# Kernel tuning notes

Hardware: AMD Instinct MI355X
Metric: run time of the kernel (lower is better)

Reference implementation:

```python
import jax, jax.numpy as jnp
import numpy as np

NORM_EPS = 1e-6

B, C, H, W = 4, 256, 48, 48
CE = 512           # C * expansion_ratio
N_STATE = 16       # Mamba d_state
DT_RANK = 32       # Ce // 16


def setup_inputs() -> dict:
    key = jax.random.key(0)
    ks = jax.random.split(key, 12)
    s = 0.02
    inp = {
        "x": jax.random.normal(ks[0], (B, C, H, W), jnp.float32),
        "norm_w": jnp.ones((C,), jnp.float32),
        "norm_b": jnp.zeros((C,), jnp.float32),
        "w_ex": jax.random.normal(ks[1], (2 * CE, C), jnp.float32) * s,
        "b_ex": jnp.zeros((2 * CE,), jnp.float32),
        "w_proj": jax.random.normal(ks[2], (C, CE), jnp.float32) * s,
        "b_proj": jnp.zeros((C,), jnp.float32),
        "dw_kernel": jax.random.normal(ks[3], (3, 3, 1, CE), jnp.float32) * 0.1,  # HWIO depthwise
        "A_log": jnp.log(jnp.broadcast_to(jnp.arange(1, N_STATE + 1, dtype=jnp.float32), (CE, N_STATE))),
        "D": jnp.ones((CE,), jnp.float32),
        "W_xproj": jax.random.normal(ks[4], (DT_RANK + 2 * N_STATE, CE), jnp.float32) * s,
        "b_xproj": jnp.zeros((DT_RANK + 2 * N_STATE,), jnp.float32),
        "W_dt": jax.random.normal(ks[5], (CE, DT_RANK), jnp.float32) * s,
        "b_dt": jnp.full((CE,), -3.0, jnp.float32),  # softplus -> small positive dt
    }
    return inp


def _forward(x, norm_w, norm_b, w_ex, b_ex, w_proj, b_proj,
             dw_kernel, A_log, D, W_xproj, b_xproj, W_dt, b_dt):
    Bt, Cc, Hh, Ww = x.shape
    Ce = dw_kernel.shape[-1]
    Ns = A_log.shape[1]
    dt_rank = W_dt.shape[1]

    # NCHW -> NHWC, LayerNorm over C
    xp = jnp.transpose(x, (0, 2, 3, 1))
    mu = xp.mean(-1, keepdims=True)
    var = xp.var(-1, keepdims=True)
    xn = (xp - mu) * jax.lax.rsqrt(var + NORM_EPS) * norm_w + norm_b

    # expansion + split
    uv = xn @ w_ex.T + b_ex                       # [B,H,W,2Ce]
    u, v = jnp.split(uv, 2, axis=-1)
    gate = u * jax.nn.sigmoid(-u)                 # r_silu(u)
    g = u * jax.nn.sigmoid(u)                     # SiLU(u)

    # depthwise 3x3 conv (NHWC) + SiLU
    v = jax.lax.conv_general_dilated(
        v, dw_kernel, window_strides=(1, 1), padding='SAME',
        dimension_numbers=('NHWC', 'HWIO', 'NHWC'), feature_group_count=Ce)
    v = v * jax.nn.sigmoid(v)

    gate = v * gate                               # fuse gate before SSM

    # ---- Mamba selective scan over raster-flattened HW sequence ----
    L = Hh * Ww
    vs = v.reshape(Bt, L, Ce)                     # [B,L,Ce]
    dbc = vs @ W_xproj.T + b_xproj                # [B,L,dt_rank+2N]
    dt = dbc[..., :dt_rank]
    Bm = dbc[..., dt_rank:dt_rank + Ns]           # [B,L,N]
    Cm = dbc[..., dt_rank + Ns:]                  # [B,L,N]
    delta = jax.nn.softplus(dt @ W_dt.T + b_dt)   # [B,L,Ce]
    A = -jnp.exp(A_log)                           # [Ce,N], negative -> stable

    def step(h, inp):
        d_t, b_t, c_t, v_t = inp                  # [B,Ce],[B,N],[B,N],[B,Ce]
        dA = jnp.exp(d_t[..., None] * A)          # [B,Ce,N]
        h = h * dA + d_t[..., None] * b_t[:, None, :] * v_t[..., None]
        y = jnp.einsum('bcn,bn->bc', h, c_t) + D * v_t
        return h, y

    h0 = jnp.zeros((Bt, Ce, Ns), x.dtype)
    seq = (jnp.swapaxes(delta, 0, 1), jnp.swapaxes(Bm, 0, 1),
           jnp.swapaxes(Cm, 0, 1), jnp.swapaxes(vs, 0, 1))
    _, ys = jax.lax.scan(step, h0, seq)           # ys: [L,B,Ce]
    y = jnp.swapaxes(ys, 0, 1).reshape(Bt, Hh, Ww, Ce)

    out = (y * g + gate) @ w_proj.T + b_proj      # [B,H,W,C]
    return jnp.transpose(out, (0, 3, 1, 2))       # NCHW


def reference(x, norm_w, norm_b, w_ex, b_ex, w_proj, b_proj,
              dw_kernel, A_log, D, W_xproj, b_xproj, W_dt, b_dt):
    return _forward(x, norm_w, norm_b, w_ex, b_ex, w_proj, b_proj,
                    dw_kernel, A_log, D, W_xproj, b_xproj, W_dt, b_dt)
```

## Files before the change

kernel.cpp:

```cpp
#include <hip/hip_runtime.h>
#include <hip/hip_bf16.h>

#define B_   4
#define C_   256
#define HH   48
#define WW   48
#define L_   2304
#define BL   9216
#define CE_  512
#define NS   16
#define DTR  32
#define NCH  72
#define CHL  32

typedef __attribute__((ext_vector_type(8))) short s16x8;
typedef __attribute__((ext_vector_type(4))) float f32x4;

__device__ __forceinline__ ushort f2bf(float f) {
  union { float f; unsigned u; } v; v.f = f;
  unsigned r = v.u + 0x7fffu + ((v.u >> 16) & 1u);
  return (ushort)(r >> 16);
}
__device__ __forceinline__ float bf2f(ushort h) {
  union { unsigned u; float f; } v; v.u = ((unsigned)h) << 16;
  return v.f;
}
__device__ __forceinline__ float lo_f(unsigned u) {
  union { unsigned u; float f; } v; v.u = u << 16; return v.f;
}
__device__ __forceinline__ float hi_f(unsigned u) {
  union { unsigned u; float f; } v; v.u = u & 0xffff0000u; return v.f;
}

__global__ __launch_bounds__(256) void prep_k(const float* __restrict__ w_ex,
                                              const float* __restrict__ w_proj,
                                              const float* __restrict__ W_xp,
                                              const float* __restrict__ b_xp,
                                              const float* __restrict__ W_dt,
                                              const float* __restrict__ b_dt,
                                              ushort* __restrict__ w_ex_bf,
                                              ushort* __restrict__ w_proj_bf,
                                              ushort* __restrict__ wcat_bf,
                                              float* __restrict__ bcat) {
  int idx = blockIdx.x * 256 + threadIdx.x;
  if (idx < 262144) {
    w_ex_bf[idx] = f2bf(w_ex[idx]);
  } else if (idx < 393216) {
    int i = idx - 262144; w_proj_bf[i] = f2bf(w_proj[i]);
  } else if (idx < 688128) {
    int i2 = idx - 393216;
    int i = i2 >> 9, j = i2 & 511;
    float s = 0.f;
    if (i < 512) {
      #pragma unroll
      for (int r = 0; r < 32; r++) s = fmaf(W_dt[i * 32 + r], W_xp[r * 512 + j], s);
    } else if (i < 544) {
      s = W_xp[(i - 480) * 512 + j];
    }
    wcat_bf[i2] = f2bf(s);
  } else if (idx < 688704) {
    int n = idx - 688128;
    float s;
    if (n < 512) {
      s = b_dt[n];
      #pragma unroll
      for (int r = 0; r < 32; r++) s = fmaf(W_dt[n * 32 + r], b_xp[r], s);
    } else if (n < 544) {
      s = b_xp[32 + (n - 512)];
    } else s = 0.f;
    bcat[n] = s;
  }
}

__global__ __launch_bounds__(256) void ln_k(const float* __restrict__ x,
                                            const float* __restrict__ w,
                                            const float* __restrict__ bia,
                                            ushort* __restrict__ xn_bf) {
  __shared__ float xt[C_][17];
  __shared__ float ps[16][17], ps2[16][17];
  __shared__ float mu_s[16], r_s[16];
  __shared__ float w_s[C_], b_s[C_];
  int blk = blockIdx.x;
  int b = blk / 144, p0 = (blk - b * 144) * 16;
  int t = threadIdx.x;
  w_s[t] = w[t]; b_s[t] = bia[t];
  #pragma unroll
  for (int it = 0; it < 16; it++) {
    int i = it * 256 + t;
    int c = i >> 4, pj = i & 15;
    xt[c][pj] = x[((size_t)(b * C_ + c)) * L_ + p0 + pj];
  }
  __syncthreads();
  {
    int ci = t >> 4, pj = t & 15;
    float s = 0.f, s2 = 0.f;
    #pragma unroll
    for (int k = 0; k < 16; k++) {
      float v = xt[ci * 16 + k][pj];
      s += v; s2 += v * v;
    }
    ps[ci][pj] = s; ps2[ci][pj] = s2;
  }
  __syncthreads();
  if (t < 16) {
    float s = 0.f, s2 = 0.f;
    #pragma unroll
    for (int ci = 0; ci < 16; ci++) { s += ps[ci][t]; s2 += ps2[ci][t]; }
    float mu = s * (1.f / C_);
    float var = s2 * (1.f / C_) - mu * mu;
    mu_s[t] = mu; r_s[t] = rsqrtf(var + 1e-6f);
  }
  __syncthreads();
  int pj = t & 15, c0 = (t >> 4) * 16;
  float mu = mu_s[pj], r = r_s[pj];
  s16x8 v0, v1;
  #pragma unroll
  for (int k = 0; k < 8; k++) {
    int c = c0 + k;
    v0[k] = (short)f2bf((xt[c][pj] - mu) * r * w_s[c] + b_s[c]);
  }
  #pragma unroll
  for (int k = 0; k < 8; k++) {
    int c = c0 + 8 + k;
    v1[k] = (short)f2bf((xt[c][pj] - mu) * r * w_s[c] + b_s[c]);
  }
  ushort* dst = xn_bf + ((size_t)(b * L_ + p0 + pj)) * C_ + c0;
  *(s16x8*)dst = v0;
  *(s16x8*)(dst + 8) = v1;
}

template<int TM, int TN, int WN, int FM, int FN, int K>
__device__ __forceinline__ void mfma_gemm(const ushort* __restrict__ A,
                                          const ushort* __restrict__ Bm,
                                          int m0, int n0, ushort* sh,
                                          f32x4 acc[FM][FN]) {
  const int t = threadIdx.x;
  const int lane = t & 63;
  const int wid = t >> 6;
  const int wm = wid / WN, wn = wid % WN;
  constexpr int ASZ = TM * 32, BSZ = TN * 32;
  #pragma unroll
  for (int i = 0; i < FM; i++)
    #pragma unroll
    for (int j = 0; j < FN; j++) acc[i][j] = (f32x4){0.f, 0.f, 0.f, 0.f};

  auto stage = [&](int kt, int buf) {
    ushort* Ad = sh + buf * (ASZ + BSZ);
    ushort* Bd = Ad + ASZ;
    #pragma unroll
    for (int ch = t; ch < TM * 4; ch += 256) {
      int k8 = ch / TM, row = ch % TM;
      const ushort* g = A + (size_t)(m0 + row) * K + kt + k8 * 8;
      __builtin_amdgcn_global_load_lds(
          (const __attribute__((address_space(1))) void*)g,
          (__attribute__((address_space(3))) void*)(Ad + (k8 * TM + row) * 8), 16, 0, 0);
    }
    #pragma unroll
    for (int ch = t; ch < TN * 4; ch += 256) {
      int k8 = ch / TN, row = ch % TN;
      const ushort* g = Bm + (size_t)(n0 + row) * K + kt + k8 * 8;
      __builtin_amdgcn_global_load_lds(
          (const __attribute__((address_space(1))) void*)g,
          (__attribute__((address_space(3))) void*)(Bd + (k8 * TN + row) * 8), 16, 0, 0);
    }
  };

  stage(0, 0);
  __syncthreads();
  constexpr int NK = K / 32;
  const int k8 = lane >> 4, r = lane & 15;
  #pragma unroll
  for (int kt = 0; kt < NK; kt++) {
    const int cur = kt & 1;
    if (kt + 1 < NK) stage((kt + 1) * 32, cur ^ 1);
    const ushort* Ab = sh + cur * (ASZ + BSZ);
    const ushort* Bb = Ab + ASZ;
    s16x8 a[FM], b[FN];
    #pragma unroll
    for (int i = 0; i < FM; i++)
      a[i] = *(const s16x8*)(Ab + (k8 * TM + wm * FM * 16 + i * 16 + r) * 8);
    #pragma unroll
    for (int j = 0; j < FN; j++)
      b[j] = *(const s16x8*)(Bb + (k8 * TN + wn * FN * 16 + j * 16 + r) * 8);
    #pragma unroll
    for (int i = 0; i < FM; i++)
      #pragma unroll
      for (int j = 0; j < FN; j++)
        acc[i][j] = __builtin_amdgcn_mfma_f32_16x16x32_bf16(a[i], b[j], acc[i][j], 0, 0, 0);
    __syncthreads();
  }
}

__global__ __launch_bounds__(256) void gemm_expand_k(const ushort* __restrict__ xn,
                                                     const ushort* __restrict__ wex,
                                                     const float* __restrict__ b_ex,
                                                     ushort* __restrict__ u_bf,
                                                     ushort* __restrict__ v_bf) {
  __shared__ __align__(16) ushort sh[128 * 136];
  f32x4 acc[4][4];
  int m0 = blockIdx.y * 128, n0 = blockIdx.x * 128;
  mfma_gemm<128, 128, 2, 4, 4, 256>(xn, wex, m0, n0, sh, acc);
  int lane = threadIdx.x & 63, wid = threadIdx.x >> 6;
  int wm = wid >> 1, wn = wid & 1;
  int q4 = (lane >> 4) * 4, cix = lane & 15;
  const int ST = 136;
  #pragma unroll
  for (int j = 0; j < 4; j++) {
    int ncl = wn * 64 + j * 16 + cix;
    float bias = b_ex[n0 + ncl];
    #pragma unroll
    for (int i = 0; i < 4; i++) {
      int ml = wm * 64 + i * 16 + q4;
      #pragma unroll
      for (int q = 0; q < 4; q++)
        sh[(ml + q) * ST + ncl] = f2bf(acc[i][j][q] + bias);
    }
  }
  __syncthreads();
  ushort* base = (n0 < 512) ? u_bf : v_bf;
  int nb = (n0 < 512) ? n0 : n0 - 512;
  int ml = threadIdx.x >> 1, nc0 = (threadIdx.x & 1) * 64;
  ushort* dst = base + (size_t)(m0 + ml) * CE_ + nb + nc0;
  const ushort* srcp = sh + ml * ST + nc0;
  #pragma unroll
  for (int k = 0; k < 8; k++)
    *(s16x8*)(dst + k * 8) = *(const s16x8*)(srcp + k * 8);
}

__global__ __launch_bounds__(256) void gemm_dbc_k(const ushort* __restrict__ vs,
                                                  const ushort* __restrict__ wcat,
                                                  const float* __restrict__ bcat,
                                                  float* __restrict__ delta,
                                                  float* __restrict__ bc) {
  __shared__ __align__(16) ushort sh[2 * (128 * 32 + 64 * 32)];
  f32x4 acc[4][2];
  int m0 = blockIdx.y * 128, n0 = blockIdx.x * 64;
  mfma_gemm<128, 64, 2, 4, 2, 512>(vs, wcat, m0, n0, sh, acc);
  int lane = threadIdx.x & 63, wid = threadIdx.x >> 6;
  int wm = wid >> 1, wn = wid & 1;
  int q4 = (lane >> 4) * 4, cix = lane & 15;
  #pragma unroll
  for (int j = 0; j < 2; j++) {
    int nc = n0 + wn * 32 + j * 16 + cix;
    if (nc >= 544) continue;
    float bias = bcat[nc];
    #pragma unroll
    for (int i = 0; i < 4; i++) {
      int mr = m0 + wm * 64 + i * 16 + q4;
      #pragma unroll
      for (int q = 0; q < 4; q++) {
        float xv = acc[i][j][q] + bias;
        if (nc < 512)
          delta[(size_t)(mr + q) * CE_ + nc] =
              fmaxf(xv, 0.f) + __logf(1.f + __expf(-fabsf(xv)));
        else
          bc[(size_t)(mr + q) * 32 + (nc - 512)] = xv;
      }
    }
  }
}

__global__ __launch_bounds__(256) void gemm_proj_k(const ushort* __restrict__ z,
                                                   const ushort* __restrict__ wpr,
                                                   const float* __restrict__ b_proj,
                                                   float* __restrict__ out) {
  __shared__ __align__(16) ushort sh[2 * (64 * 32 + 64 * 32)];
  __shared__ float Cs[64][65];
  f32x4 acc[2][2];
  int m0 = blockIdx.y * 64, n0 = blockIdx.x * 64;
  mfma_gemm<64, 64, 2, 2, 2, 512>(z, wpr, m0, n0, sh, acc);
  int t = threadIdx.x;
  int lane = t & 63, wid = t >> 6;
  int wm = wid >> 1, wn = wid & 1;
  int q4 = (lane >> 4) * 4, cix = lane & 15;
  #pragma unroll
  for (int j = 0; j < 2; j++)
    #pragma unroll
    for (int i = 0; i < 2; i++)
      #pragma unroll
      for (int q = 0; q < 4; q++)
        Cs[wm * 32 + i * 16 + q4 + q][wn * 32 + j * 16 + cix] = acc[i][j][q];
  __syncthreads();
  int nc_l = t >> 2, p4 = (t & 3) * 16;
  float bias = b_proj[n0 + nc_l];
  int pix0 = m0 + p4;
  int bb = pix0 / L_, p = pix0 - bb * L_;
  float* dst = out + ((size_t)(bb * C_ + n0 + nc_l)) * L_ + p;
  #pragma unroll
  for (int k = 0; k < 4; k++) {
    float4 vv = make_float4(Cs[p4 + k * 4 + 0][nc_l] + bias,
                            Cs[p4 + k * 4 + 1][nc_l] + bias,
                            Cs[p4 + k * 4 + 2][nc_l] + bias,
                            Cs[p4 + k * 4 + 3][nc_l] + bias);
    *(float4*)(dst + k * 4) = vv;
  }
}

__global__ __launch_bounds__(256) void dwconv_k(const ushort* __restrict__ vraw,
                                                const float* __restrict__ kw,
                                                ushort* __restrict__ vs) {
  int p = blockIdx.x * 2 + (threadIdx.x >> 7);
  int b = p / L_, q = p - b * L_;
  int y = q / WW, x = q - y * WW;
  int c4 = (threadIdx.x & 127) * 4;
  float a0 = 0.f, a1 = 0.f, a2 = 0.f, a3 = 0.f;
  #pragma unroll
  for (int ky = 0; ky < 3; ky++) {
    int yy = y + ky - 1;
    if (yy < 0 || yy >= HH) continue;
    #pragma unroll
    for (int kx = 0; kx < 3; kx++) {
      int xx = x + kx - 1;
      if (xx < 0 || xx >= WW) continue;
      uint2 pv = *(const uint2*)(vraw + ((size_t)(b * L_ + yy * WW + xx)) * CE_ + c4);
      float4 kk = *(const float4*)(kw + (ky * 3 + kx) * CE_ + c4);
      a0 = fmaf(lo_f(pv.x), kk.x, a0);
      a1 = fmaf(hi_f(pv.x), kk.y, a1);
      a2 = fmaf(lo_f(pv.y), kk.z, a2);
      a3 = fmaf(hi_f(pv.y), kk.w, a3);
    }
  }
  float s0 = a0 / (1.f + __expf(-a0));
  float s1 = a1 / (1.f + __expf(-a1));
  float s2 = a2 / (1.f + __expf(-a2));
  float s3 = a3 / (1.f + __expf(-a3));
  uint2 outp;
  outp.x = (unsigned)f2bf(s0) | ((unsigned)f2bf(s1) << 16);
  outp.y = (unsigned)f2bf(s2) | ((unsigned)f2bf(s3) << 16);
  *(uint2*)(vs + (size_t)p * CE_ + c4) = outp;
}

__global__ __launch_bounds__(256) void scan1_k(const float* __restrict__ delta,
                                               const float* __restrict__ bc,
                                               const ushort* __restrict__ vs,
                                               const float* __restrict__ A_log,
                                               float* __restrict__ S,
                                               float* __restrict__ Dsum) {
  __shared__ float bt_s[CHL * NS];
  int b = blockIdx.z, ch = blockIdx.y;
  int c = blockIdx.x * 256 + threadIdx.x;
  int mbase = b * L_ + ch * CHL;
  for (int i = threadIdx.x; i < CHL * NS; i += 256)
    bt_s[i] = bc[(size_t)(mbase + (i >> 4)) * 32 + (i & 15)];
  __syncthreads();
  float Ac[NS], h[NS];
  #pragma unroll
  for (int n = 0; n < NS; n++) {
    Ac[n] = -__expf(A_log[c * NS + n]);
    h[n] = 0.f;
  }
  float dsum = 0.f;
  for (int t = 0; t < CHL; t++) {
    int m = mbase + t;
    float d  = delta[(size_t)m * CE_ + c];
    float vv = bf2f(vs[(size_t)m * CE_ + c]);
    float dv = d * vv;
    dsum += d;
    #pragma unroll
    for (int n = 0; n < NS; n++)
      h[n] = fmaf(h[n], __expf(d * Ac[n]), dv * bt_s[t * NS + n]);
  }
  size_t sidx = (size_t)(b * NCH + ch) * CE_ + c;
  #pragma unroll
  for (int n = 0; n < NS; n++) S[sidx * NS + n] = h[n];
  Dsum[sidx] = dsum;
}

__global__ __launch_bounds__(256) void scan2_k(const float* __restrict__ A_log,
                                               float* __restrict__ S,
                                               const float* __restrict__ Dsum) {
  int idx = blockIdx.x * 256 + threadIdx.x;
  int n = idx & 15, c = (idx >> 4) & (CE_ - 1), b = idx >> 13;
  float Ac = -__expf(A_log[c * NS + n]);
  float h = 0.f;
  for (int ch = 0; ch < NCH; ch++) {
    size_t sidx = (size_t)(b * NCH + ch) * CE_ + c;
    float sv = S[sidx * NS + n];
    float ds = Dsum[sidx];
    S[sidx * NS + n] = h;
    h = fmaf(h, __expf(Ac * ds), sv);
  }
}

__global__ __launch_bounds__(256) void scan3_k(const float* __restrict__ delta,
                                               const float* __restrict__ bc,
                                               const ushort* __restrict__ vs,
                                               const float* __restrict__ A_log,
                                               const float* __restrict__ Dv,
                                               const float* __restrict__ hstart,
                                               const ushort* __restrict__ u,
                                               ushort* __restrict__ z) {
  __shared__ float bc_s[CHL * 32];
  int b = blockIdx.z, ch = blockIdx.y;
  int c = blockIdx.x * 256 + threadIdx.x;
  int mbase = b * L_ + ch * CHL;
  for (int i = threadIdx.x; i < CHL * 32; i += 256)
    bc_s[i] = bc[(size_t)(mbase + (i >> 5)) * 32 + (i & 31)];
  __syncthreads();
  size_t sidx = (size_t)(b * NCH + ch) * CE_ + c;
  float Ac[NS], h[NS];
  #pragma unroll
  for (int n = 0; n < NS; n++) {
    Ac[n] = -__expf(A_log[c * NS + n]);
    h[n] = hstart[sidx * NS + n];
  }
  float Dc = Dv[c];
  for (int t = 0; t < CHL; t++) {
    int m = mbase + t;
    float d  = delta[(size_t)m * CE_ + c];
    float vv = bf2f(vs[(size_t)m * CE_ + c]);
    float dv = d * vv;
    float y = 0.f;
    #pragma unroll
    for (int n = 0; n < NS; n++) {
      h[n] = fmaf(h[n], __expf(d * Ac[n]), dv * bc_s[t * 32 + n]);
      y = fmaf(h[n], bc_s[t * 32 + 16 + n], y);
    }
    y = fmaf(Dc, vv, y);
    float uu = bf2f(u[(size_t)m * CE_ + c]);
    float s  = 1.f / (1.f + __expf(-uu));
    z[(size_t)m * CE_ + c] = f2bf(uu * (y * s + vv * (1.f - s)));
  }
}

extern "C" void kernel_launch(void* const* d_in, const int* in_sizes, int n_in,
                              void* d_out, int out_size, void* d_ws, size_t ws_size,
                              hipStream_t stream) {
  const float* x      = (const float*)d_in[0];
  const float* norm_w = (const float*)d_in[1];
  const float* norm_b = (const float*)d_in[2];
  const float* w_ex   = (const float*)d_in[3];
  const float* b_ex   = (const float*)d_in[4];
  const float* w_proj = (const float*)d_in[5];
  const float* b_proj = (const float*)d_in[6];
  const float* dw_k   = (const float*)d_in[7];
  const float* A_log  = (const float*)d_in[8];
  const float* Dv     = (const float*)d_in[9];
  const float* W_xp   = (const float*)d_in[10];
  const float* b_xp   = (const float*)d_in[11];
  const float* W_dt   = (const float*)d_in[12];
  const float* b_dt   = (const float*)d_in[13];
  float* out = (float*)d_out;

  char* wsb = (char*)d_ws;
  size_t off = 0;
  auto alloc = [&](size_t bytes) { void* p = wsb + off; off += (bytes + 255) & ~(size_t)255; return p; };
  ushort* u_bf    = (ushort*)alloc((size_t)BL * CE_ * 2);
  ushort* vraw_bf = (ushort*)alloc((size_t)BL * CE_ * 2);
  ushort* vs_bf   = (ushort*)alloc((size_t)BL * CE_ * 2);
  ushort* xn_bf   = (ushort*)alloc((size_t)BL * C_ * 2);
  float*  delta   = (float*)alloc((size_t)BL * CE_ * 4);
  float*  bc      = (float*)alloc((size_t)BL * 32 * 4);
  float*  S       = (float*)alloc((size_t)B_ * NCH * CE_ * NS * 4);
  float*  Dsum    = (float*)alloc((size_t)B_ * NCH * CE_ * 4);
  ushort* w_ex_bf = (ushort*)alloc((size_t)2 * CE_ * C_ * 2);
  ushort* w_pr_bf = (ushort*)alloc((size_t)C_ * CE_ * 2);
  ushort* wcat_bf = (ushort*)alloc((size_t)576 * CE_ * 2);
  float*  bcat    = (float*)alloc((size_t)576 * 4);
  ushort* z_bf = vraw_bf;

  prep_k<<<2691, 256, 0, stream>>>(w_ex, w_proj, W_xp, b_xp, W_dt, b_dt,
                                   w_ex_bf, w_pr_bf, wcat_bf, bcat);
  ln_k<<<576, 256, 0, stream>>>(x, norm_w, norm_b, xn_bf);
  gemm_expand_k<<<dim3(8, 72), 256, 0, stream>>>(xn_bf, w_ex_bf, b_ex, u_bf, vraw_bf);
  dwconv_k<<<BL / 2, 256, 0, stream>>>(vraw_bf, dw_k, vs_bf);
  gemm_dbc_k<<<dim3(9, 72), 256, 0, stream>>>(vs_bf, wcat_bf, bcat, delta, bc);
  scan1_k<<<dim3(2, NCH, B_), 256, 0, stream>>>(delta, bc, vs_bf, A_log, S, Dsum);
  scan2_k<<<128, 256, 0, stream>>>(A_log, S, Dsum);
  scan3_k<<<dim3(2, NCH, B_), 256, 0, stream>>>(delta, bc, vs_bf, A_log, Dv, S, u_bf, z_bf);
  gemm_proj_k<<<dim3(4, 144), 256, 0, stream>>>(z_bf, w_pr_bf, b_proj, out);
}
```

Measured before the change: 245.6 us.

## Fuse LN with weight prep, bf16 delta, smem-tiled dwconv, swap GEMM grid order

Merges the weight-conversion kernel and the LayerNorm kernel into one launch, and vectorises the LayerNorm loads with float4. Stores delta as bf16, staged through shared memory for coalesced writes, which halves delta traffic in both scan passes; the scan loops are partially unrolled. Rewrites the depthwise conv to stage three input rows and the kernel taps in shared memory per output row. Also swaps the GEMM grid dimensions so M tiles vary fastest. Storing delta in bf16 costs precision in the SSM recurrence.

```diff
diff --git a/kernel.cpp b/kernel.cpp
--- a/kernel.cpp
+++ b/kernel.cpp
@@ -32,101 +32,103 @@
   union { unsigned u; float f; } v; v.u = u & 0xffff0000u; return v.f;
 }
 
-__global__ __launch_bounds__(256) void prep_k(const float* __restrict__ w_ex,
-                                              const float* __restrict__ w_proj,
-                                              const float* __restrict__ W_xp,
-                                              const float* __restrict__ b_xp,
-                                              const float* __restrict__ W_dt,
-                                              const float* __restrict__ b_dt,
-                                              ushort* __restrict__ w_ex_bf,
-                                              ushort* __restrict__ w_proj_bf,
-                                              ushort* __restrict__ wcat_bf,
-                                              float* __restrict__ bcat) {
-  int idx = blockIdx.x * 256 + threadIdx.x;
-  if (idx < 262144) {
-    w_ex_bf[idx] = f2bf(w_ex[idx]);
-  } else if (idx < 393216) {
-    int i = idx - 262144; w_proj_bf[i] = f2bf(w_proj[i]);
-  } else if (idx < 688128) {
-    int i2 = idx - 393216;
-    int i = i2 >> 9, j = i2 & 511;
-    float s = 0.f;
-    if (i < 512) {
-      #pragma unroll
-      for (int r = 0; r < 32; r++) s = fmaf(W_dt[i * 32 + r], W_xp[r * 512 + j], s);
-    } else if (i < 544) {
-      s = W_xp[(i - 480) * 512 + j];
-    }
-    wcat_bf[i2] = f2bf(s);
-  } else if (idx < 688704) {
-    int n = idx - 688128;
-    float s;
-    if (n < 512) {
-      s = b_dt[n];
-      #pragma unroll
-      for (int r = 0; r < 32; r++) s = fmaf(W_dt[n * 32 + r], b_xp[r], s);
-    } else if (n < 544) {
-      s = b_xp[32 + (n - 512)];
-    } else s = 0.f;
-    bcat[n] = s;
-  }
-}
-
-__global__ __launch_bounds__(256) void ln_k(const float* __restrict__ x,
-                                            const float* __restrict__ w,
-                                            const float* __restrict__ bia,
-                                            ushort* __restrict__ xn_bf) {
-  __shared__ float xt[C_][17];
-  __shared__ float ps[16][17], ps2[16][17];
-  __shared__ float mu_s[16], r_s[16];
-  __shared__ float w_s[C_], b_s[C_];
-  int blk = blockIdx.x;
-  int b = blk / 144, p0 = (blk - b * 144) * 16;
+__global__ __launch_bounds__(256) void lnprep_k(const float* __restrict__ x,
+                                                const float* __restrict__ w,
+                                                const float* __restrict__ bia,
+                                                ushort* __restrict__ xn_bf,
+                                                const float* __restrict__ w_ex,
+                                                const float* __restrict__ w_proj,
+                                                const float* __restrict__ W_xp,
+                                                const float* __restrict__ b_xp,
+                                                const float* __restrict__ W_dt,
+                                                const float* __restrict__ b_dt,
+                                                ushort* __restrict__ w_ex_bf,
+                                                ushort* __restrict__ w_proj_bf,
+                                                ushort* __restrict__ wcat_bf,
+                                                float* __restrict__ bcat) {
   int t = threadIdx.x;
-  w_s[t] = w[t]; b_s[t] = bia[t];
-  #pragma unroll
-  for (int it = 0; it < 16; it++) {
-    int i = it * 256 + t;
-    int c = i >> 4, pj = i & 15;
-    xt[c][pj] = x[((size_t)(b * C_ + c)) * L_ + p0 + pj];
-  }
-  __syncthreads();
-  {
-    int ci = t >> 4, pj = t & 15;
-    float s = 0.f, s2 = 0.f;
-    #pragma unroll
-    for (int k = 0; k < 16; k++) {
-      float v = xt[ci * 16 + k][pj];
-      s += v; s2 += v * v;
-    }
-    ps[ci][pj] = s; ps2[ci][pj] = s2;
-  }
-  __syncthreads();
-  if (t < 16) {
-    float s = 0.f, s2 = 0.f;
-    #pragma unroll
-    for (int ci = 0; ci < 16; ci++) { s += ps[ci][t]; s2 += ps2[ci][t]; }
-    float mu = s * (1.f / C_);
-    float var = s2 * (1.f / C_) - mu * mu;
-    mu_s[t] = mu; r_s[t] = rsqrtf(var + 1e-6f);
-  }
-  __syncthreads();
-  int pj = t & 15, c0 = (t >> 4) * 16;
-  float mu = mu_s[pj], r = r_s[pj];
-  s16x8 v0, v1;
-  #pragma unroll
-  for (int k = 0; k < 8; k++) {
-    int c = c0 + k;
-    v0[k] = (short)f2bf((xt[c][pj] - mu) * r * w_s[c] + b_s[c]);
-  }
-  #pragma unroll
-  for (int k = 0; k < 8; k++) {
-    int c = c0 + 8 + k;
-    v1[k] = (short)f2bf((xt[c][pj] - mu) * r * w_s[c] + b_s[c]);
-  }
-  ushort* dst = xn_bf + ((size_t)(b * L_ + p0 + pj)) * C_ + c0;
-  *(s16x8*)dst = v0;
-  *(s16x8*)(dst + 8) = v1;
+  if (blockIdx.x < 576) {
+    __shared__ float xt[C_][17];
+    __shared__ float ps[16][17], ps2[16][17];
+    __shared__ float mu_s[16], r_s[16];
+    __shared__ float w_s[C_], b_s[C_];
+    int blk = blockIdx.x;
+    int b = blk / 144, p0 = (blk - b * 144) * 16;
+    w_s[t] = w[t]; b_s[t] = bia[t];
+    #pragma unroll
+    for (int it = 0; it < 4; it++) {
+      int i = it * 1024 + t * 4;
+      int c = i >> 4, pj = i & 15;
+      float4 v = *(const float4*)&x[((size_t)(b * C_ + c)) * L_ + p0 + pj];
+      xt[c][pj] = v.x; xt[c][pj + 1] = v.y; xt[c][pj + 2] = v.z; xt[c][pj + 3] = v.w;
+    }
+    __syncthreads();
+    {
+      int ci = t >> 4, pj = t & 15;
+      float s = 0.f, s2 = 0.f;
+      #pragma unroll
+      for (int k = 0; k < 16; k++) {
+        float v = xt[ci * 16 + k][pj];
+        s += v; s2 += v * v;
+      }
+      ps[ci][pj] = s; ps2[ci][pj] = s2;
+    }
+    __syncthreads();
+    if (t < 16) {
+      float s = 0.f, s2 = 0.f;
+      #pragma unroll
+      for (int ci = 0; ci < 16; ci++) { s += ps[ci][t]; s2 += ps2[ci][t]; }
+      float mu = s * (1.f / C_);
+      float var = s2 * (1.f / C_) - mu * mu;
+      mu_s[t] = mu; r_s[t] = rsqrtf(var + 1e-6f);
+    }
+    __syncthreads();
+    int pj = t & 15, c0 = (t >> 4) * 16;
+    float mu = mu_s[pj], r = r_s[pj];
+    s16x8 v0, v1;
+    #pragma unroll
+    for (int k = 0; k < 8; k++) {
+      int c = c0 + k;
+      v0[k] = (short)f2bf((xt[c][pj] - mu) * r * w_s[c] + b_s[c]);
+    }
+    #pragma unroll
+    for (int k = 0; k < 8; k++) {
+      int c = c0 + 8 + k;
+      v1[k] = (short)f2bf((xt[c][pj] - mu) * r * w_s[c] + b_s[c]);
+    }
+    ushort* dst = xn_bf + ((size_t)(b * L_ + p0 + pj)) * C_ + c0;
+    *(s16x8*)dst = v0;
+    *(s16x8*)(dst + 8) = v1;
+  } else {
+    int idx = (blockIdx.x - 576) * 256 + t;
+    if (idx < 262144) {
+      w_ex_bf[idx] = f2bf(w_ex[idx]);
+    } else if (idx < 393216) {
+      int i = idx - 262144; w_proj_bf[i] = f2bf(w_proj[i]);
+    } else if (idx < 688128) {
+      int i2 = idx - 393216;
+      int i = i2 >> 9, j = i2 & 511;
+      float s = 0.f;
+      if (i < 512) {
+        #pragma unroll
+        for (int r = 0; r < 32; r++) s = fmaf(W_dt[i * 32 + r], W_xp[r * 512 + j], s);
+      } else if (i < 544) {
+        s = W_xp[(i - 480) * 512 + j];
+      }
+      wcat_bf[i2] = f2bf(s);
+    } else if (idx < 688704) {
+      int n = idx - 688128;
+      float s;
+      if (n < 512) {
+        s = b_dt[n];
+        #pragma unroll
+        for (int r = 0; r < 32; r++) s = fmaf(W_dt[n * 32 + r], b_xp[r], s);
+      } else if (n < 544) {
+        s = b_xp[32 + (n - 512)];
+      } else s = 0.f;
+      bcat[n] = s;
+    }
+  }
 }
 
 template<int TM, int TN, int WN, int FM, int FN, int K>
@@ -198,7 +200,7 @@
                                                      ushort* __restrict__ v_bf) {
   __shared__ __align__(16) ushort sh[128 * 136];
   f32x4 acc[4][4];
-  int m0 = blockIdx.y * 128, n0 = blockIdx.x * 128;
+  int m0 = blockIdx.x * 128, n0 = blockIdx.y * 128;
   mfma_gemm<128, 128, 2, 4, 4, 256>(xn, wex, m0, n0, sh, acc);
   int lane = threadIdx.x & 63, wid = threadIdx.x >> 6;
   int wm = wid >> 1, wn = wid & 1;
@@ -230,31 +232,51 @@
 __global__ __launch_bounds__(256) void gemm_dbc_k(const ushort* __restrict__ vs,
                                                   const ushort* __restrict__ wcat,
                                                   const float* __restrict__ bcat,
-                                                  float* __restrict__ delta,
+                                                  ushort* __restrict__ delta,
                                                   float* __restrict__ bc) {
   __shared__ __align__(16) ushort sh[2 * (128 * 32 + 64 * 32)];
   f32x4 acc[4][2];
-  int m0 = blockIdx.y * 128, n0 = blockIdx.x * 64;
+  int m0 = blockIdx.x * 128, n0 = blockIdx.y * 64;
   mfma_gemm<128, 64, 2, 4, 2, 512>(vs, wcat, m0, n0, sh, acc);
   int lane = threadIdx.x & 63, wid = threadIdx.x >> 6;
   int wm = wid >> 1, wn = wid & 1;
   int q4 = (lane >> 4) * 4, cix = lane & 15;
-  #pragma unroll
-  for (int j = 0; j < 2; j++) {
-    int nc = n0 + wn * 32 + j * 16 + cix;
-    if (nc >= 544) continue;
-    float bias = bcat[nc];
-    #pragma unroll
-    for (int i = 0; i < 4; i++) {
-      int mr = m0 + wm * 64 + i * 16 + q4;
-      #pragma unroll
-      for (int q = 0; q < 4; q++) {
-        float xv = acc[i][j][q] + bias;
-        if (nc < 512)
-          delta[(size_t)(mr + q) * CE_ + nc] =
-              fmaxf(xv, 0.f) + __logf(1.f + __expf(-fabsf(xv)));
-        else
-          bc[(size_t)(mr + q) * 32 + (nc - 512)] = xv;
+  if (n0 < 512) {
+    const int ST = 72;
+    #pragma unroll
+    for (int j = 0; j < 2; j++) {
+      int ncl = wn * 32 + j * 16 + cix;
+      float bias = bcat[n0 + ncl];
+      #pragma unroll
+      for (int i = 0; i < 4; i++) {
+        int ml = wm * 64 + i * 16 + q4;
+        #pragma unroll
+        for (int q = 0; q < 4; q++) {
+          float xv = acc[i][j][q] + bias;
+          float sp = fmaxf(xv, 0.f) + __logf(1.f + __expf(-fabsf(xv)));
+          sh[(ml + q) * ST + ncl] = f2bf(sp);
+        }
+      }
+    }
+    __syncthreads();
+    int ml = threadIdx.x >> 1, h32 = (threadIdx.x & 1) * 32;
+    ushort* dst = delta + (size_t)(m0 + ml) * CE_ + n0 + h32;
+    const ushort* srcp = sh + ml * ST + h32;
+    #pragma unroll
+    for (int k = 0; k < 4; k++)
+      *(s16x8*)(dst + k * 8) = *(const s16x8*)(srcp + k * 8);
+  } else {
+    #pragma unroll
+    for (int j = 0; j < 2; j++) {
+      int nc = n0 + wn * 32 + j * 16 + cix;
+      if (nc >= 544) continue;
+      float bias = bcat[nc];
+      #pragma unroll
+      for (int i = 0; i < 4; i++) {
+        int mr = m0 + wm * 64 + i * 16 + q4;
+        #pragma unroll
+        for (int q = 0; q < 4; q++)
+          bc[(size_t)(mr + q) * 32 + (nc - 512)] = acc[i][j][q] + bias;
       }
     }
   }
@@ -267,7 +289,7 @@
   __shared__ __align__(16) ushort sh[2 * (64 * 32 + 64 * 32)];
   __shared__ float Cs[64][65];
   f32x4 acc[2][2];
-  int m0 = blockIdx.y * 64, n0 = blockIdx.x * 64;
+  int m0 = blockIdx.x * 64, n0 = blockIdx.y * 64;
   mfma_gemm<64, 64, 2, 2, 2, 512>(z, wpr, m0, n0, sh, acc);
   int t = threadIdx.x;
   int lane = t & 63, wid = t >> 6;
@@ -299,38 +321,57 @@
 __global__ __launch_bounds__(256) void dwconv_k(const ushort* __restrict__ vraw,
                                                 const float* __restrict__ kw,
                                                 ushort* __restrict__ vs) {
-  int p = blockIdx.x * 2 + (threadIdx.x >> 7);
-  int b = p / L_, q = p - b * L_;
-  int y = q / WW, x = q - y * WW;
-  int c4 = (threadIdx.x & 127) * 4;
-  float a0 = 0.f, a1 = 0.f, a2 = 0.f, a3 = 0.f;
-  #pragma unroll
-  for (int ky = 0; ky < 3; ky++) {
-    int yy = y + ky - 1;
-    if (yy < 0 || yy >= HH) continue;
-    #pragma unroll
-    for (int kx = 0; kx < 3; kx++) {
-      int xx = x + kx - 1;
-      if (xx < 0 || xx >= WW) continue;
-      uint2 pv = *(const uint2*)(vraw + ((size_t)(b * L_ + yy * WW + xx)) * CE_ + c4);
-      float4 kk = *(const float4*)(kw + (ky * 3 + kx) * CE_ + c4);
-      a0 = fmaf(lo_f(pv.x), kk.x, a0);
-      a1 = fmaf(hi_f(pv.x), kk.y, a1);
-      a2 = fmaf(lo_f(pv.y), kk.z, a2);
-      a3 = fmaf(hi_f(pv.y), kk.w, a3);
-    }
-  }
-  float s0 = a0 / (1.f + __expf(-a0));
-  float s1 = a1 / (1.f + __expf(-a1));
-  float s2 = a2 / (1.f + __expf(-a2));
-  float s3 = a3 / (1.f + __expf(-a3));
-  uint2 outp;
-  outp.x = (unsigned)f2bf(s0) | ((unsigned)f2bf(s1) << 16);
-  outp.y = (unsigned)f2bf(s2) | ((unsigned)f2bf(s3) << 16);
-  *(uint2*)(vs + (size_t)p * CE_ + c4) = outp;
-}
-
-__global__ __launch_bounds__(256) void scan1_k(const float* __restrict__ delta,
+  __shared__ ushort rows[3][WW][128];
+  __shared__ float kws[9][128];
+  int y = blockIdx.x, cg = blockIdx.y, b = blockIdx.z;
+  int t = threadIdx.x;
+  int cbase = cg * 128;
+  for (int i = t; i < 3 * WW * 32; i += 256) {
+    int ry = i / (WW * 32);
+    int rem = i - ry * WW * 32;
+    int xx = rem >> 5, c8 = rem & 31;
+    int yy = y + ry - 1;
+    uint2 val = make_uint2(0u, 0u);
+    if (yy >= 0 && yy < HH)
+      val = *(const uint2*)(vraw + ((size_t)(b * L_ + yy * WW + xx)) * CE_ + cbase + c8 * 4);
+    *(uint2*)&rows[ry][xx][c8 * 4] = val;
+  }
+  for (int i = t; i < 9 * 32; i += 256) {
+    int tap = i >> 5, c8 = i & 31;
+    *(float4*)&kws[tap][c8 * 4] = *(const float4*)(kw + tap * CE_ + cbase + c8 * 4);
+  }
+  __syncthreads();
+  int xg = t >> 5, c8 = t & 31;
+  #pragma unroll
+  for (int xi = 0; xi < 6; xi++) {
+    int x = xg * 6 + xi;
+    float a0 = 0.f, a1 = 0.f, a2 = 0.f, a3 = 0.f;
+    #pragma unroll
+    for (int ky = 0; ky < 3; ky++) {
+      #pragma unroll
+      for (int kx = 0; kx < 3; kx++) {
+        int xx = x + kx - 1;
+        if (xx < 0 || xx >= WW) continue;
+        uint2 pv = *(const uint2*)&rows[ky][xx][c8 * 4];
+        float4 kk = *(const float4*)&kws[ky * 3 + kx][c8 * 4];
+        a0 = fmaf(lo_f(pv.x), kk.x, a0);
+        a1 = fmaf(hi_f(pv.x), kk.y, a1);
+        a2 = fmaf(lo_f(pv.y), kk.z, a2);
+        a3 = fmaf(hi_f(pv.y), kk.w, a3);
+      }
+    }
+    float s0 = a0 / (1.f + __expf(-a0));
+    float s1 = a1 / (1.f + __expf(-a1));
+    float s2 = a2 / (1.f + __expf(-a2));
+    float s3 = a3 / (1.f + __expf(-a3));
+    uint2 outp;
+    outp.x = (unsigned)f2bf(s0) | ((unsigned)f2bf(s1) << 16);
+    outp.y = (unsigned)f2bf(s2) | ((unsigned)f2bf(s3) << 16);
+    *(uint2*)(vs + ((size_t)(b * L_ + y * WW + x)) * CE_ + cbase + c8 * 4) = outp;
+  }
+}
+
+__global__ __launch_bounds__(256) void scan1_k(const ushort* __restrict__ delta,
                                                const float* __restrict__ bc,
                                                const ushort* __restrict__ vs,
                                                const float* __restrict__ A_log,
@@ -350,9 +391,10 @@
     h[n] = 0.f;
   }
   float dsum = 0.f;
+  #pragma unroll 4
   for (int t = 0; t < CHL; t++) {
     int m = mbase + t;
-    float d  = delta[(size_t)m * CE_ + c];
+    float d  = bf2f(delta[(size_t)m * CE_ + c]);
     float vv = bf2f(vs[(size_t)m * CE_ + c]);
     float dv = d * vv;
     dsum += d;
@@ -382,7 +424,7 @@
   }
 }
 
-__global__ __launch_bounds__(256) void scan3_k(const float* __restrict__ delta,
+__global__ __launch_bounds__(256) void scan3_k(const ushort* __restrict__ delta,
                                                const float* __restrict__ bc,
                                                const ushort* __restrict__ vs,
                                                const float* __restrict__ A_log,
@@ -405,9 +447,10 @@
     h[n] = hstart[sidx * NS + n];
   }
   float Dc = Dv[c];
+  #pragma unroll 4
   for (int t = 0; t < CHL; t++) {
     int m = mbase + t;
-    float d  = delta[(size_t)m * CE_ + c];
+    float d  = bf2f(delta[(size_t)m * CE_ + c]);
     float vv = bf2f(vs[(size_t)m * CE_ + c]);
     float dv = d * vv;
     float y = 0.f;
@@ -449,7 +492,7 @@
   ushort* vraw_bf = (ushort*)alloc((size_t)BL * CE_ * 2);
   ushort* vs_bf   = (ushort*)alloc((size_t)BL * CE_ * 2);
   ushort* xn_bf   = (ushort*)alloc((size_t)BL * C_ * 2);
-  float*  delta   = (float*)alloc((size_t)BL * CE_ * 4);
+  ushort* delta   = (ushort*)alloc((size_t)BL * CE_ * 2);
   float*  bc      = (float*)alloc((size_t)BL * 32 * 4);
   float*  S       = (float*)alloc((size_t)B_ * NCH * CE_ * NS * 4);
   float*  Dsum    = (float*)alloc((size_t)B_ * NCH * CE_ * 4);
@@ -459,14 +502,14 @@
   float*  bcat    = (float*)alloc((size_t)576 * 4);
   ushort* z_bf = vraw_bf;
 
-  prep_k<<<2691, 256, 0, stream>>>(w_ex, w_proj, W_xp, b_xp, W_dt, b_dt,
-                                   w_ex_bf, w_pr_bf, wcat_bf, bcat);
-  ln_k<<<576, 256, 0, stream>>>(x, norm_w, norm_b, xn_bf);
-  gemm_expand_k<<<dim3(8, 72), 256, 0, stream>>>(xn_bf, w_ex_bf, b_ex, u_bf, vraw_bf);
-  dwconv_k<<<BL / 2, 256, 0, stream>>>(vraw_bf, dw_k, vs_bf);
-  gemm_dbc_k<<<dim3(9, 72), 256, 0, stream>>>(vs_bf, wcat_bf, bcat, delta, bc);
+  lnprep_k<<<576 + 2691, 256, 0, stream>>>(x, norm_w, norm_b, xn_bf,
+                                           w_ex, w_proj, W_xp, b_xp, W_dt, b_dt,
+                                           w_ex_bf, w_pr_bf, wcat_bf, bcat);
+  gemm_expand_k<<<dim3(72, 8), 256, 0, stream>>>(xn_bf, w_ex_bf, b_ex, u_bf, vraw_bf);
+  dwconv_k<<<dim3(HH, 4, B_), 256, 0, stream>>>(vraw_bf, dw_k, vs_bf);
+  gemm_dbc_k<<<dim3(72, 9), 256, 0, stream>>>(vs_bf, wcat_bf, bcat, delta, bc);
   scan1_k<<<dim3(2, NCH, B_), 256, 0, stream>>>(delta, bc, vs_bf, A_log, S, Dsum);
   scan2_k<<<128, 256, 0, stream>>>(A_log, S, Dsum);
   scan3_k<<<dim3(2, NCH, B_), 256, 0, stream>>>(delta, bc, vs_bf, A_log, Dv, S, u_bf, z_bf);
-  gemm_proj_k<<<dim3(4, 144), 256, 0, stream>>>(z_bf, w_pr_bf, b_proj, out);
-}
+  gemm_proj_k<<<dim3(144, 4), 256, 0, stream>>>(z_bf, w_pr_bf, b_proj, out);
+}
```

New measurement: 232.8 us. 5.2% less time.
